# Kernel tuning notes

Hardware: AMD Instinct MI355X
Metric: run time of the kernel (lower is better)

The kernel has to match this reference:

```python
import jax, jax.numpy as jnp
import numpy as np

B, T, D, K = 4, 4096, 256, 16


def hankel_eigvecs(T: int, k: int) -> jnp.ndarray:
    """Top-k |eigenvalue| eigenvectors of Z_ij = 2/((i+j)^3 - (i+j)), 1-indexed."""
    idx = np.arange(1, T + 1, dtype=np.float64)
    ij = idx[None, :] + idx[:, None]
    Z = 2.0 / (ij ** 3 - ij)
    w, v = np.linalg.eigh(Z)
    top = np.argsort(-np.abs(w))[:k]
    return jnp.asarray(v[:, top], dtype=jnp.float32)  # (T, K)


def setup_inputs() -> dict:
    key = jax.random.key(0)
    kx, kw = jax.random.split(key)
    x = jax.random.normal(kx, (B, T, D), dtype=jnp.float32)
    # Stacked weights of the K independent nn.Linear(D, D, bias=False) modules.
    # W[k] is the torch Linear weight (out, in); y = c @ W[k].T.
    W = jax.random.normal(kw, (K, D, D), dtype=jnp.float32) * (1.0 / np.sqrt(D))
    phi = hankel_eigvecs(T, K)  # Hankel eigenvector buffer (non-trainable)
    return {"x": x, "W": W, "phi": phi}


def reference(x, W, phi):
    # x: (B,T,D), W: (K,D,D), phi: (T,K)
    # c_k[t] = cumsum_{s<=t} phi[s,k] * x[s]   -> batched over all K filters
    C = jnp.cumsum(phi[None, :, :, None] * x[:, :, None, :], axis=1)  # (B,T,K,D)
    # out[t] = sum_k phi[t,k] * (c_k[t] @ W_k^T)
    out = jnp.einsum('btkd,ked,tk->bte', C, W, phi)  # (B,T,D)
    return out  # dropout is identity in eval mode (dropout=0.0)
```

## Files before the change

### kernel.cpp

```cpp
#include <hip/hip_runtime.h>


typedef __bf16 bf16x8 __attribute__((ext_vector_type(8)));
typedef float  f32x4  __attribute__((ext_vector_type(4)));
typedef unsigned short u16;

__device__ static inline u16 f2bf(float f) {
    unsigned int u = __float_as_uint(f);
    u = (u + 0x7fffu + ((u >> 16) & 1u)) >> 16;
    return (u16)u;
}

__device__ static inline void gload16(const void* g, void* l) {
    __builtin_amdgcn_global_load_lds((const __attribute__((address_space(1))) void*)g,
                                     (__attribute__((address_space(3))) void*)l, 16, 0, 0);
}

__global__ __launch_bounds__(256) void k0_wt(const float* __restrict__ W, u16* __restrict__ WT) {
    const int e = blockIdx.x, d = threadIdx.x;
    union { u16 u[16]; uint4 v[2]; } ob;
#pragma unroll
    for (int k = 0; k < 16; ++k)
        ob.u[k] = f2bf(W[((size_t)k * 256 + e) * 256 + d]);
    uint4* dst = (uint4*)(WT + (size_t)e * 4096 + d * 16);
    dst[0] = ob.v[0]; dst[1] = ob.v[1];
}

__global__ __launch_bounds__(256) void k1_sums(const float* __restrict__ x,
                                               const float* __restrict__ phi,
                                               float* __restrict__ U) {
    __shared__ float phis[256];
    const int tid = threadIdx.x;
    const int b = blockIdx.x, c = blockIdx.y;
    const int t0 = c * 16;
    phis[tid] = phi[t0 * 16 + tid];
    __syncthreads();
    float acc[16];
#pragma unroll
    for (int k = 0; k < 16; ++k) acc[k] = 0.f;
    for (int s = 0; s < 16; ++s) {
        const float xv = x[(size_t)((b << 12) + t0 + s) * 256 + tid];
        union { float f[16]; float4 v[4]; } pv;
#pragma unroll
        for (int j = 0; j < 4; ++j) pv.v[j] = *(const float4*)&phis[s * 16 + j * 4];
#pragma unroll
        for (int k = 0; k < 16; ++k) acc[k] = fmaf(pv.f[k], xv, acc[k]);
    }
    float4* Up = (float4*)(U + ((size_t)((b * 256 + c) * 256 + tid)) * 16);
    union { float f[16]; float4 v[4]; } ov;
#pragma unroll
    for (int k = 0; k < 16; ++k) ov.f[k] = acc[k];
#pragma unroll
    for (int j = 0; j < 4; ++j) Up[j] = ov.v[j];
}

__global__ __launch_bounds__(256) void k2_scan(float* __restrict__ U) {
    const int b = blockIdx.x;
    const int dk = blockIdx.y * 256 + threadIdx.x;
    float* base = U + (size_t)b * 1048576 + dk;
    float runv = 0.f;
    for (int g = 0; g < 16; ++g) {
        float v[16];
#pragma unroll
        for (int j = 0; j < 16; ++j) v[j] = base[(size_t)(g * 16 + j) * 4096];
#pragma unroll
        for (int j = 0; j < 16; ++j) {
            const float t = v[j];
            base[(size_t)(g * 16 + j) * 4096] = runv;
            runv += t;
        }
    }
}

__global__ __launch_bounds__(512, 4) void k4_fused(const float* __restrict__ x,
                                                   const float* __restrict__ phi,
                                                   const float* __restrict__ U,
                                                   const u16* __restrict__ BT,
                                                   float* __restrict__ C) {
    __shared__ __align__(16) char smem[81920];
    const int tid = threadIdx.x;
    const int m0 = blockIdx.x * 64;
    const int ks = blockIdx.y;
    const int b  = m0 >> 12, t0 = m0 & 4095, c0 = t0 >> 4;
    const int w = tid >> 6, l = tid & 63;
    const int wm = (w >> 2) * 32, wn = (w & 3) * 64;
    const int lg = l >> 4, lr = l & 15;
    f32x4 acc[2][4] = {};

    float p[16];
    if (w < 4) {
#pragma unroll
        for (int s = 0; s < 16; ++s) p[s] = phi[(t0 + w * 16 + s) * 16 + lr];
    }
    const char* Bb = (const char*)BT;
    const int tl = tid & 255;
    const int colb = (lg * 16 + lr) * 2;

    auto stageB = [&](int kt, int buf) {
        const int kofs = ks * 4096 + kt * 128;
#pragma unroll
        for (int c = 0; c < 8; ++c) {
            const int row = c * 32 + (tl >> 3);
            gload16(Bb + (size_t)row * 8192 + kofs + (((tl & 7) * 16) ^ ((row & 7) << 4)),
                    smem + 16384 + buf * 32768 + c * 4096 + tl * 16);
        }
    };
    auto chains = [&](int kt, int buf) {
        const int d = ks * 128 + kt * 4 + lg;
        float run = U[(((size_t)(b * 256 + c0 + w)) * 256 + d) * 16 + lr];
        char* Ab = smem + buf * 8192 + w * 2048;
#pragma unroll
        for (int s = 0; s < 16; ++s) {
            const float xv = x[(size_t)(m0 + w * 16 + s) * 256 + d];
            run = fmaf(p[s], xv, run);
            *(u16*)(Ab + s * 128 + (colb ^ ((s & 7) << 4))) = f2bf(p[s] * run);
        }
    };

    if (w >= 4) stageB(0, 0); else chains(0, 0);
    __syncthreads();

    for (int kt = 0; kt < 32; ++kt) {
        const int cur = kt & 1;
        if (kt < 31) {
            if (w >= 4) stageB(kt + 1, cur ^ 1);
            else        chains(kt + 1, cur ^ 1);
        }
        const char* Abase = smem + cur * 8192;
        const char* Bbase = smem + 16384 + cur * 32768;
#pragma unroll
        for (int kk = 0; kk < 2; ++kk) {
            const int kb = kk * 64 + lg * 16;
            bf16x8 af[2], bfv[4];
#pragma unroll
            for (int mi = 0; mi < 2; ++mi) {
                const int r = wm + mi * 16 + lr;
                af[mi] = *(const bf16x8*)(Abase + r * 128 + (kb ^ ((r & 7) << 4)));
            }
#pragma unroll
            for (int ni = 0; ni < 4; ++ni) {
                const int n = wn + ni * 16 + lr;
                bfv[ni] = *(const bf16x8*)(Bbase + n * 128 + (kb ^ ((n & 7) << 4)));
            }
#pragma unroll
            for (int mi = 0; mi < 2; ++mi)
#pragma unroll
                for (int ni = 0; ni < 4; ++ni)
                    acc[mi][ni] = __builtin_amdgcn_mfma_f32_16x16x32_bf16(af[mi], bfv[ni], acc[mi][ni], 0, 0, 0);
        }
        __syncthreads();
    }

#pragma unroll
    for (int mi = 0; mi < 2; ++mi)
#pragma unroll
        for (int ni = 0; ni < 4; ++ni)
#pragma unroll
            for (int r = 0; r < 4; ++r) {
                const int row = m0 + wm + mi * 16 + lg * 4 + r;
                const int col = wn + ni * 16 + lr;
                unsafeAtomicAdd(&C[(size_t)row * 256 + col], acc[mi][ni][r]);
            }
}

extern "C" void kernel_launch(void* const* d_in, const int* in_sizes, int n_in,
                              void* d_out, int out_size, void* d_ws, size_t ws_size,
                              hipStream_t stream) {
    const float* x   = (const float*)d_in[0];
    const float* W   = (const float*)d_in[1];
    const float* phi = (const float*)d_in[2];
    float* out = (float*)d_out;

    char* ws = (char*)d_ws;
    u16*   WT = (u16*)ws;
    float* U  = (float*)(ws + (2u << 20));

    k0_wt  <<<256, 256, 0, stream>>>(W, WT);
    k1_sums<<<dim3(4, 256), 256, 0, stream>>>(x, phi, U);
    k2_scan<<<dim3(4, 16), 256, 0, stream>>>(U);
    hipMemsetAsync(d_out, 0, (size_t)out_size * sizeof(float), stream);
    k4_fused<<<dim3(256, 2), 512, 0, stream>>>(x, phi, U, WT, out);
}
```

Baseline: 99.89 us.

## Prefetch x/U chain inputs two steps ahead and widen scan grid

The fused GEMM kernel now loads x and U values for the producer warps into registers two k-steps ahead, using ping-pong register sets. The loop is unrolled by two so the A-tile build no longer stalls on global loads within each step. The bf16 conversion switches from manual rounding to a native cast. The scan kernel launches 64-thread blocks over more blocks to spread its work across more CUs. The trade-off is higher register pressure from 32 extra floats per producer thread.

```diff
diff --git a/kernel.cpp b/kernel.cpp
--- a/kernel.cpp
+++ b/kernel.cpp
@@ -54,9 +54,9 @@
     for (int j = 0; j < 4; ++j) Up[j] = ov.v[j];
 }
 
-__global__ __launch_bounds__(256) void k2_scan(float* __restrict__ U) {
+__global__ __launch_bounds__(64) void k2_scan(float* __restrict__ U) {
     const int b = blockIdx.x;
-    const int dk = blockIdx.y * 256 + threadIdx.x;
+    const int dk = blockIdx.y * 64 + threadIdx.x;
     float* base = U + (size_t)b * 1048576 + dk;
     float runv = 0.f;
     for (int g = 0; g < 16; ++g) {
@@ -87,14 +87,15 @@
     const int lg = l >> 4, lr = l & 15;
     f32x4 acc[2][4] = {};
 
+    const int dl = lg, kl = lr;
+    const int cb = (dl * 16 + kl) * 2;
     float p[16];
     if (w < 4) {
 #pragma unroll
-        for (int s = 0; s < 16; ++s) p[s] = phi[(t0 + w * 16 + s) * 16 + lr];
+        for (int s = 0; s < 16; ++s) p[s] = phi[(t0 + w * 16 + s) * 16 + kl];
     }
     const char* Bb = (const char*)BT;
     const int tl = tid & 255;
-    const int colb = (lg * 16 + lr) * 2;
 
     auto stageB = [&](int kt, int buf) {
         const int kofs = ks * 4096 + kt * 128;
@@ -105,29 +106,25 @@
                     smem + 16384 + buf * 32768 + c * 4096 + tl * 16);
         }
     };
-    auto chains = [&](int kt, int buf) {
-        const int d = ks * 128 + kt * 4 + lg;
-        float run = U[(((size_t)(b * 256 + c0 + w)) * 256 + d) * 16 + lr];
-        char* Ab = smem + buf * 8192 + w * 2048;
+    auto issue = [&](float (&xr)[16], float& us, int kt) {
+        const int d = ks * 128 + kt * 4 + dl;
+        const float* xp = x + (size_t)(m0 + w * 16) * 256 + d;
+#pragma unroll
+        for (int s = 0; s < 16; ++s) xr[s] = xp[(size_t)s * 256];
+        us = U[(((size_t)(b * 256 + c0 + w)) * 256 + d) * 16 + kl];
+    };
+    auto chains = [&](const float (&xr)[16], float us, int buf) {
+        float run = us;
+        char* Ab = smem + buf * 8192 + (w * 16) * 128;
 #pragma unroll
         for (int s = 0; s < 16; ++s) {
-            const float xv = x[(size_t)(m0 + w * 16 + s) * 256 + d];
-            run = fmaf(p[s], xv, run);
-            *(u16*)(Ab + s * 128 + (colb ^ ((s & 7) << 4))) = f2bf(p[s] * run);
-        }
-    };
-
-    if (w >= 4) stageB(0, 0); else chains(0, 0);
-    __syncthreads();
-
-    for (int kt = 0; kt < 32; ++kt) {
-        const int cur = kt & 1;
-        if (kt < 31) {
-            if (w >= 4) stageB(kt + 1, cur ^ 1);
-            else        chains(kt + 1, cur ^ 1);
-        }
-        const char* Abase = smem + cur * 8192;
-        const char* Bbase = smem + 16384 + cur * 32768;
+            run = fmaf(p[s], xr[s], run);
+            *(__bf16*)(Ab + s * 128 + (cb ^ ((s & 7) << 4))) = (__bf16)(p[s] * run);
+        }
+    };
+    auto mfma_phase = [&](int buf) {
+        const char* Abase = smem + buf * 8192;
+        const char* Bbase = smem + 16384 + buf * 32768;
 #pragma unroll
         for (int kk = 0; kk < 2; ++kk) {
             const int kb = kk * 64 + lg * 16;
@@ -148,6 +145,37 @@
                 for (int ni = 0; ni < 4; ++ni)
                     acc[mi][ni] = __builtin_amdgcn_mfma_f32_16x16x32_bf16(af[mi], bfv[ni], acc[mi][ni], 0, 0, 0);
         }
+    };
+
+    float xA[16], xB[16], uA, uB;
+    if (w < 4) {
+        issue(xA, uA, 0); issue(xB, uB, 1);
+        chains(xA, uA, 0);
+    } else {
+        stageB(0, 0);
+    }
+    __syncthreads();
+
+    for (int it = 0; it < 16; ++it) {
+        const int kt0 = 2 * it;
+        if (w < 4) {
+            if (kt0 + 2 < 32) issue(xA, uA, kt0 + 2);
+            chains(xB, uB, 1);
+        } else {
+            stageB(kt0 + 1, 1);
+        }
+        mfma_phase(0);
+        __syncthreads();
+        const int kt1 = kt0 + 1;
+        if (kt1 + 1 < 32) {
+            if (w < 4) {
+                if (kt1 + 2 < 32) issue(xB, uB, kt1 + 2);
+                chains(xA, uA, 0);
+            } else {
+                stageB(kt1 + 1, 0);
+            }
+        }
+        mfma_phase(1);
         __syncthreads();
     }
 
@@ -177,7 +205,7 @@
 
     k0_wt  <<<256, 256, 0, stream>>>(W, WT);
     k1_sums<<<dim3(4, 256), 256, 0, stream>>>(x, phi, U);
-    k2_scan<<<dim3(4, 16), 256, 0, stream>>>(U);
+    k2_scan<<<dim3(4, 64), 64, 0, stream>>>(U);
     hipMemsetAsync(d_out, 0, (size_t)out_size * sizeof(float), stream);
     k4_fused<<<dim3(256, 2), 512, 0, stream>>>(x, phi, U, WT, out);
 }
```

After: 113.3 us. +13.4%, slower.

## Spread chain compute and B staging across all warps, overlap loads with MFMA

Applied to the files above, without the earlier changes.

The fused kernel no longer splits warps into producer (A-chain) and loader (B stage) roles. All 8 warps now issue the B global-to-LDS loads and compute half-length 8-step prefix chains, joined with a cross-lane shuffle. The x/U loads for the next tile are issued before the MFMA phase and the chain compute runs after it, so latency is hidden behind matrix math. The scan kernel also moves to 64-thread blocks to put more blocks in flight. The cost is extra registers and shuffle work in every warp.

```diff
diff --git a/kernel.cpp b/kernel.cpp
--- a/kernel.cpp
+++ b/kernel.cpp
@@ -54,9 +54,9 @@
     for (int j = 0; j < 4; ++j) Up[j] = ov.v[j];
 }
 
-__global__ __launch_bounds__(256) void k2_scan(float* __restrict__ U) {
+__global__ __launch_bounds__(64) void k2_scan(float* __restrict__ U) {
     const int b = blockIdx.x;
-    const int dk = blockIdx.y * 256 + threadIdx.x;
+    const int dk = blockIdx.y * 64 + threadIdx.x;
     float* base = U + (size_t)b * 1048576 + dk;
     float runv = 0.f;
     for (int g = 0; g < 16; ++g) {
@@ -87,47 +87,50 @@
     const int lg = l >> 4, lr = l & 15;
     f32x4 acc[2][4] = {};
 
-    float p[16];
-    if (w < 4) {
+    const int ch = w & 3, khi = w >> 2;
+    const int klo = l & 7, dl = (l >> 3) & 3, sh = l >> 5;
+    const int kl = khi * 8 + klo;
+    const int row0 = ch * 16 + sh * 8;
+    const int colb = (dl * 16 + kl) * 2;
+
+    float p[8];
 #pragma unroll
-        for (int s = 0; s < 16; ++s) p[s] = phi[(t0 + w * 16 + s) * 16 + lr];
-    }
+    for (int s = 0; s < 8; ++s) p[s] = phi[(t0 + row0 + s) * 16 + kl];
+
     const char* Bb = (const char*)BT;
-    const int tl = tid & 255;
-    const int colb = (lg * 16 + lr) * 2;
+    float xr[8], useed;
 
+    auto bload = [&](int kt) {
+        const int d = ks * 128 + kt * 4 + dl;
+        const float* xp = x + (size_t)(m0 + row0) * 256 + d;
+#pragma unroll
+        for (int s = 0; s < 8; ++s) xr[s] = xp[(size_t)s * 256];
+        useed = U[(((size_t)(b * 256 + c0 + ch)) * 256 + d) * 16 + kl];
+    };
     auto stageB = [&](int kt, int buf) {
         const int kofs = ks * 4096 + kt * 128;
 #pragma unroll
-        for (int c = 0; c < 8; ++c) {
-            const int row = c * 32 + (tl >> 3);
-            gload16(Bb + (size_t)row * 8192 + kofs + (((tl & 7) * 16) ^ ((row & 7) << 4)),
-                    smem + 16384 + buf * 32768 + c * 4096 + tl * 16);
+        for (int c = 0; c < 4; ++c) {
+            const int row = c * 64 + (tid >> 3);
+            gload16(Bb + (size_t)row * 8192 + kofs + (((tid & 7) * 16) ^ ((row & 7) << 4)),
+                    smem + 16384 + buf * 32768 + c * 8192 + tid * 16);
         }
     };
-    auto chains = [&](int kt, int buf) {
-        const int d = ks * 128 + kt * 4 + lg;
-        float run = U[(((size_t)(b * 256 + c0 + w)) * 256 + d) * 16 + lr];
-        char* Ab = smem + buf * 8192 + w * 2048;
+    auto bcomp = [&](int buf) {
+        float run = sh ? 0.f : useed;
+        float ap[8];
 #pragma unroll
-        for (int s = 0; s < 16; ++s) {
-            const float xv = x[(size_t)(m0 + w * 16 + s) * 256 + d];
-            run = fmaf(p[s], xv, run);
-            *(u16*)(Ab + s * 128 + (colb ^ ((s & 7) << 4))) = f2bf(p[s] * run);
-        }
+        for (int s = 0; s < 8; ++s) { run = fmaf(p[s], xr[s], run); ap[s] = run; }
+        const float cross = __shfl_xor(run, 32, 64);
+        const float base = sh ? cross : 0.f;
+        char* Ab = smem + buf * 8192 + row0 * 128;
+#pragma unroll
+        for (int s = 0; s < 8; ++s)
+            *(__bf16*)(Ab + s * 128 + (colb ^ (s << 4))) = (__bf16)(p[s] * (ap[s] + base));
     };
-
-    if (w >= 4) stageB(0, 0); else chains(0, 0);
-    __syncthreads();
-
-    for (int kt = 0; kt < 32; ++kt) {
-        const int cur = kt & 1;
-        if (kt < 31) {
-            if (w >= 4) stageB(kt + 1, cur ^ 1);
-            else        chains(kt + 1, cur ^ 1);
-        }
-        const char* Abase = smem + cur * 8192;
-        const char* Bbase = smem + 16384 + cur * 32768;
+    auto mfma_phase = [&](int buf) {
+        const char* Abase = smem + buf * 8192;
+        const char* Bbase = smem + 16384 + buf * 32768;
 #pragma unroll
         for (int kk = 0; kk < 2; ++kk) {
             const int kb = kk * 64 + lg * 16;
@@ -148,6 +151,19 @@
                 for (int ni = 0; ni < 4; ++ni)
                     acc[mi][ni] = __builtin_amdgcn_mfma_f32_16x16x32_bf16(af[mi], bfv[ni], acc[mi][ni], 0, 0, 0);
         }
+    };
+
+    bload(0); stageB(0, 0); bcomp(0);
+    __syncthreads();
+
+    for (int kt = 0; kt < 32; ++kt) {
+        const int cur = kt & 1;
+        if (kt < 31) {
+            bload(kt + 1);
+            stageB(kt + 1, cur ^ 1);
+        }
+        mfma_phase(cur);
+        if (kt < 31) bcomp(cur ^ 1);
         __syncthreads();
     }
 
@@ -177,7 +193,7 @@
 
     k0_wt  <<<256, 256, 0, stream>>>(W, WT);
     k1_sums<<<dim3(4, 256), 256, 0, stream>>>(x, phi, U);
-    k2_scan<<<dim3(4, 16), 256, 0, stream>>>(U);
+    k2_scan<<<dim3(4, 64), 64, 0, stream>>>(U);
     hipMemsetAsync(d_out, 0, (size_t)out_size * sizeof(float), stream);
     k4_fused<<<dim3(256, 2), 512, 0, stream>>>(x, phi, U, WT, out);
 }
```

New measurement: 103.0 us. 3.1% more time.
